# Performance work log

Measured on AMD Instinct MI355X. Metric: run time of the kernel, lower is better.

Reference implementation:

```python
import jax, jax.numpy as jnp
import numpy as np

B, T, C, H, W = 2, 4, 3, 96, 96
HF, L = 128, 6
TC = T * C
EPS = 1e-5


def swish(x):
    return x * jax.nn.sigmoid(x)


def _build_edges(h, w):
    # self-loops + 8-neighbor grid edges, exactly as image_to_graph
    edges = [np.stack([np.arange(h * w)] * 2)]
    nx0, ny0 = np.meshgrid(np.arange(w), np.arange(h), indexing='ij')
    for dx, dy in [(-1, -1), (0, -1), (1, -1), (-1, 0), (1, 0), (-1, 1), (0, 1), (1, 1)]:
        nx, ny = nx0 + dx, ny0 + dy
        src = ny * w + nx
        dst = (ny - dy) * w + (nx - dx)
        ok = (nx >= 0) & (nx < w) & (0 <= ny) & (ny < h)
        edges.append(np.stack([src[ok], dst[ok]]))
    return np.concatenate(edges, axis=1)


def setup_inputs() -> dict:
    key = jax.random.key(0)
    ks = iter(jax.random.split(key, 40))

    def lin(fi, fo):
        return jax.random.normal(next(ks), (fi, fo), jnp.float32) / np.sqrt(fi).astype(np.float32)

    x = jax.random.normal(next(ks), (B, T, C, H, W), jnp.float32)
    ei = _build_edges(H, W)
    px, py = np.meshgrid(np.arange(W), np.arange(H), indexing='ij')
    pos = np.stack([px.flatten(), py.flatten()], 1).astype(np.float32) / (H - 1)
    return dict(
        x=x,
        edge_src=jnp.asarray(ei[0], jnp.int32),
        edge_dst=jnp.asarray(ei[1], jnp.int32),
        pos=jnp.asarray(pos),
        emb_w1=lin(TC + 2, HF), emb_b1=jnp.zeros((HF,), jnp.float32),
        emb_w2=lin(HF, HF), emb_b2=jnp.zeros((HF,), jnp.float32),
        msg_w1=jnp.stack([lin(2 * HF + TC + 1, HF) for _ in range(L)]),
        msg_b1=jnp.zeros((L, HF), jnp.float32),
        msg_w2=jnp.stack([lin(HF, HF) for _ in range(L)]),
        msg_b2=jnp.zeros((L, HF), jnp.float32),
        upd_w1=jnp.stack([lin(2 * HF, HF) for _ in range(L)]),
        upd_b1=jnp.zeros((L, HF), jnp.float32),
        upd_w2=jnp.stack([lin(HF, HF) for _ in range(L)]),
        upd_b2=jnp.zeros((L, HF), jnp.float32),
        out_w1=lin(HF, HF), out_b1=jnp.zeros((HF,), jnp.float32),
        out_w2=lin(HF, C), out_b2=jnp.zeros((C,), jnp.float32),
    )


def _forward(x, emb_w1, emb_b1, emb_w2, emb_b2, msg_w1, msg_b1, msg_w2, msg_b2,
             upd_w1, upd_b1, upd_w2, upd_b2, out_w1, out_b1, out_w2, out_b2,
             edge_src, edge_dst, pos):
    b, t, c, h, w = x.shape
    n = h * w
    u = x.reshape(b, t * c, n).transpose(0, 2, 1)                       # [B,N,TC]
    node_in = jnp.concatenate([u, jnp.broadcast_to(pos, (b, n, 2))], -1)
    hf = swish(swish(node_in @ emb_w1 + emb_b1) @ emb_w2 + emb_b2)      # [B,N,HF]
    dist = jnp.linalg.norm(pos[edge_dst] - pos[edge_src], axis=1, keepdims=True)  # [E,1]
    dist_b = jnp.broadcast_to(dist, (b,) + dist.shape)
    deg = jnp.zeros((n,), x.dtype).at[edge_dst].add(1.0)                # >=1 (self loops)
    for l in range(msg_w1.shape[0]):
        m_in = jnp.concatenate([hf[:, edge_dst], hf[:, edge_src],
                                u[:, edge_dst] - u[:, edge_src], dist_b], -1)
        m = swish(swish(m_in @ msg_w1[l] + msg_b1[l]) @ msg_w2[l] + msg_b2[l])
        agg = jnp.zeros(hf.shape, hf.dtype).at[:, edge_dst].add(m) / deg[None, :, None]
        upd = swish(swish(jnp.concatenate([hf, agg], -1) @ upd_w1[l] + upd_b1[l])
                    @ upd_w2[l] + upd_b2[l])
        hf = hf + upd                                                    # residual (in==out)
        mu = hf.mean(axis=1, keepdims=True)                              # InstanceNorm per graph
        var = hf.var(axis=1, keepdims=True)
        hf = (hf - mu) * jax.lax.rsqrt(var + EPS)
    hg = hf.reshape(b, h, w, -1)
    diff = (swish(hg @ out_w1 + out_b1) @ out_w2 + out_b2).transpose(0, 3, 1, 2)
    return (x[:, -1] + diff)[:, None]                                    # [B,1,C,H,W]


def reference(x, edge_src, edge_dst, pos, emb_w1, emb_b1, emb_w2, emb_b2,
              msg_w1, msg_b1, msg_w2, msg_b2, upd_w1, upd_b1, upd_w2, upd_b2,
              out_w1, out_b1, out_w2, out_b2):
    return _forward(x, emb_w1, emb_b1, emb_w2, emb_b2, msg_w1, msg_b1, msg_w2, msg_b2,
                    upd_w1, upd_b1, upd_w2, upd_b2, out_w1, out_b1, out_w2, out_b2,
                    edge_src, edge_dst, pos)
```

## Files before the change

kernel.cpp:

```cpp
#include <hip/hip_runtime.h>
#include <math.h>

#define HF 128
#define NB 9216
#define BB 2
#define MROWS (BB*NB)
#define GH 96
#define GW 96
#define LAYERS 6

typedef __attribute__((ext_vector_type(8))) short bf16x8;
typedef __attribute__((ext_vector_type(4))) float f32x4;

#define MFMA16(a, b, c) __builtin_amdgcn_mfma_f32_16x16x32_bf16(a, b, c, 0, 0, 0)

__device__ __forceinline__ float swishf(float x) {
    return __fdividef(x, 1.0f + __expf(-x));
}

__device__ __forceinline__ unsigned short f2b(float f) {
    unsigned u = __float_as_uint(f);
    unsigned r = (u + 0x7fffu + ((u >> 16) & 1u)) >> 16;
    return (unsigned short)r;
}
__device__ __forceinline__ float b2f(unsigned short u) {
    return __uint_as_float((unsigned)u << 16);
}

__global__ void k_prep(const float* __restrict__ embw2, const float* __restrict__ outw1,
                       const float* __restrict__ msgw1, const float* __restrict__ msgw2,
                       const float* __restrict__ updw1, const float* __restrict__ updw2,
                       unsigned short* __restrict__ wT) {
    int s = blockIdx.x;
    const float* src;
    if (s == 0) src = embw2;
    else if (s == 1) src = outw1;
    else {
        int l = (s - 2) / 6, r = (s - 2) % 6;
        if (r == 0)      src = msgw1 + (size_t)l * 269 * HF;
        else if (r == 1) src = msgw1 + (size_t)l * 269 * HF + HF * HF;
        else if (r == 2) src = msgw2 + (size_t)l * HF * HF;
        else if (r == 3) src = updw1 + (size_t)l * 256 * HF;
        else if (r == 4) src = updw1 + (size_t)l * 256 * HF + HF * HF;
        else             src = updw2 + (size_t)l * HF * HF;
    }
    __shared__ float tile[128][133];
    int t = threadIdx.x;
#pragma unroll
    for (int i = 0; i < 64; ++i) {
        int id = i * 256 + t;
        tile[id >> 7][id & 127] = src[id];
    }
    __syncthreads();
    unsigned short* o = wT + (size_t)s * 16384;
#pragma unroll
    for (int i = 0; i < 64; ++i) {
        int id = i * 256 + t;
        int col = id >> 7, k = id & 127;
        o[id] = f2b(tile[k][col]);
    }
}

__global__ void k_build(const float* __restrict__ x, const float* __restrict__ pos,
                        float* __restrict__ nodein) {
    int idx = blockIdx.x * 256 + threadIdx.x;
    if (idx >= MROWS) return;
    int b = idx / NB, n = idx - b * NB;
    float* o = nodein + (size_t)idx * 16;
    const float* xb = x + (size_t)b * 12 * NB + n;
#pragma unroll
    for (int k = 0; k < 12; ++k) o[k] = xb[(size_t)k * NB];
    o[12] = pos[2 * n];
    o[13] = pos[2 * n + 1];
    o[14] = 0.0f; o[15] = 0.0f;
}

__global__ __launch_bounds__(256, 4)
void k_emb(const float* __restrict__ nodein, const float* __restrict__ w1,
           const float* __restrict__ b1, const unsigned short* __restrict__ wT2,
           const float* __restrict__ b2,
           float* __restrict__ hf, unsigned short* __restrict__ hfb) {
    __shared__ float xs[16][14];
    __shared__ char t1s[4096];
    int t = threadIdx.x;
    int rt = blockIdx.x * 16;
    if (t < 224) {
        int r = t / 14, k = t - r * 14;
        xs[r][k] = nodein[(size_t)(rt + r) * 16 + k];
    }
    __syncthreads();
    {
        int f = t & 127, rblk = t >> 7;
        float wreg[14];
#pragma unroll
        for (int k = 0; k < 14; ++k) wreg[k] = w1[k * HF + f];
        float bv = b1[f];
#pragma unroll
        for (int i = 0; i < 8; ++i) {
            int row = rblk * 8 + i;
            float acc = bv;
#pragma unroll
            for (int k = 0; k < 14; ++k) acc = fmaf(xs[row][k], wreg[k], acc);
            int addr = (row * 256 + f * 2) ^ ((row & 7) << 4);
            *(unsigned short*)(t1s + addr) = f2b(swishf(acc));
        }
    }
    __syncthreads();
    int wave = t >> 6, lane = t & 63, lr = lane & 15, lg = lane >> 4;
    int fb = wave * 32;
    f32x4 acc[2];
    acc[0] = (f32x4)0.0f; acc[1] = (f32x4)0.0f;
#pragma unroll
    for (int kc = 0; kc < 4; ++kc) {
        int k0 = kc * 32 + lg * 8;
        bf16x8 a = *(const bf16x8*)(t1s + ((lr * 256 + k0 * 2) ^ ((lr & 7) << 4)));
#pragma unroll
        for (int j = 0; j < 2; ++j) {
            bf16x8 b = *(const bf16x8*)(wT2 + (size_t)(fb + j * 16 + lr) * HF + k0);
            acc[j] = MFMA16(a, b, acc[j]);
        }
    }
#pragma unroll
    for (int j = 0; j < 2; ++j) {
        int f = fb + j * 16 + lr;
        float bv = b2[f];
#pragma unroll
        for (int r = 0; r < 4; ++r) {
            size_t o = (size_t)(rt + lg * 4 + r) * HF + f;
            float v = swishf(acc[j][r] + bv);
            hf[o] = v;
            hfb[o] = f2b(v);
        }
    }
}

__global__ __launch_bounds__(256, 4)
void k_as(const unsigned short* __restrict__ hfb, const unsigned short* __restrict__ wA,
          const unsigned short* __restrict__ wB, const float* __restrict__ nodein,
          const float* __restrict__ w1u,
          unsigned short* __restrict__ A, unsigned short* __restrict__ S) {
    __shared__ float w1s[12][128];
    int t = threadIdx.x, wave = t >> 6, lane = t & 63, lr = lane & 15, lg = lane >> 4;
    int rt = blockIdx.x * 16;
    int fb = wave * 32;
    for (int i = t; i < 12 * 128; i += 256) w1s[i >> 7][i & 127] = w1u[i];
    f32x4 accA[2], accS[2];
    accA[0] = (f32x4)0.0f; accA[1] = (f32x4)0.0f;
    accS[0] = (f32x4)0.0f; accS[1] = (f32x4)0.0f;
#pragma unroll
    for (int kc = 0; kc < 4; ++kc) {
        int k0 = kc * 32 + lg * 8;
        bf16x8 a = *(const bf16x8*)(hfb + (size_t)(rt + lr) * HF + k0);
#pragma unroll
        for (int j = 0; j < 2; ++j) {
            bf16x8 bA = *(const bf16x8*)(wA + (size_t)(fb + j * 16 + lr) * HF + k0);
            accA[j] = MFMA16(a, bA, accA[j]);
            bf16x8 bS = *(const bf16x8*)(wB + (size_t)(fb + j * 16 + lr) * HF + k0);
            accS[j] = MFMA16(a, bS, accS[j]);
        }
    }
    float ni[4][12];
#pragma unroll
    for (int r = 0; r < 4; ++r) {
        const float4* np = (const float4*)(nodein + (size_t)(rt + lg * 4 + r) * 16);
        float4 v0 = np[0], v1 = np[1], v2 = np[2];
        ni[r][0] = v0.x; ni[r][1] = v0.y; ni[r][2] = v0.z; ni[r][3] = v0.w;
        ni[r][4] = v1.x; ni[r][5] = v1.y; ni[r][6] = v1.z; ni[r][7] = v1.w;
        ni[r][8] = v2.x; ni[r][9] = v2.y; ni[r][10] = v2.z; ni[r][11] = v2.w;
    }
    __syncthreads();
#pragma unroll
    for (int j = 0; j < 2; ++j) {
        int f = fb + j * 16 + lr;
        float au[4] = {0.f, 0.f, 0.f, 0.f};
#pragma unroll
        for (int k = 0; k < 12; ++k) {
            float wv = w1s[k][f];
#pragma unroll
            for (int r = 0; r < 4; ++r) au[r] = fmaf(ni[r][k], wv, au[r]);
        }
#pragma unroll
        for (int r = 0; r < 4; ++r) {
            size_t o = (size_t)(rt + lg * 4 + r) * HF + f;
            A[o] = f2b(accA[j][r] + au[r]);
            S[o] = f2b(accS[j][r] - au[r]);
        }
    }
}

__global__ __launch_bounds__(256, 4)
void k_agg(const unsigned short* __restrict__ Ab, const unsigned short* __restrict__ Sb,
           const unsigned short* __restrict__ wT2, const float* __restrict__ b2,
           const float* __restrict__ b1, const float* __restrict__ w1d,
           unsigned short* __restrict__ aggb) {
    __shared__ float dsb[3][128];
    __shared__ char exb[9 * 4096];
    int t = threadIdx.x, kq = t >> 6, lane = t & 63, lr = lane & 15, lg = lane >> 4;
    int bx = blockIdx.x;
    int b = bx / (NB / 16), tile = bx % (NB / 16);
    int rt = tile * 16;
    int fb = kq * 32;
    size_t bN = (size_t)b * NB;
    int R = rt / GW, C0 = rt % GW;

    if (t < 128) {
        float bb = b1[t], wd = w1d[t];
        dsb[0][t] = bb;
        dsb[1][t] = fmaf(1.0f / 95.0f, wd, bb);
        dsb[2][t] = fmaf(1.4142135623730951f / 95.0f, wd, bb);
    }
    bf16x8 w2f[2][4];
#pragma unroll
    for (int j = 0; j < 2; ++j)
#pragma unroll
        for (int kc = 0; kc < 4; ++kc)
            w2f[j][kc] = *(const bf16x8*)(wT2 + (size_t)(fb + j * 16 + lr) * HF
                                          + kc * 32 + lg * 8);
    int rowA = rt + lr;
    float Af[8];
    {
        bf16x8 av = *(const bf16x8*)(Ab + (bN + rowA) * HF + kq * 32 + lg * 8);
#pragma unroll
        for (int e = 0; e < 8; ++e) Af[e] = b2f((unsigned short)av[e]);
    }
    float b2r[2] = { b2[fb + lr], b2[fb + 16 + lr] };
    int lofs = lane * 16;
    __syncthreads();

    bf16x8 sv;
    {
        int src = min(max(rowA - 97, 0), NB - 1);
        sv = *(const bf16x8*)(Sb + (bN + src) * HF + kq * 32 + lg * 8);
    }
#pragma unroll
    for (int off = 0; off < 9; ++off) {
        int dr = off / 3 - 1, dc = off % 3 - 1;
        int dd = dr * dr + dc * dc;
        bf16x8 cur = sv;
        if (off < 8) {
            int no = off + 1;
            int dnn = (no / 3 - 1) * GW + (no % 3 - 1);
            int src = min(max(rowA + dnn, 0), NB - 1);
            sv = *(const bf16x8*)(Sb + (bN + src) * HF + kq * 32 + lg * 8);
        }
        const float* dp = &dsb[dd][kq * 32 + lg * 8];
        union { bf16x8 v; unsigned u[4]; } az;
#pragma unroll
        for (int q = 0; q < 4; ++q) {
            float zl = swishf(Af[2 * q]     + b2f((unsigned short)cur[2 * q])     + dp[2 * q]);
            float zh = swishf(Af[2 * q + 1] + b2f((unsigned short)cur[2 * q + 1]) + dp[2 * q + 1]);
            az.u[q] = (unsigned)f2b(zl) | ((unsigned)f2b(zh) << 16);
        }
        *(bf16x8*)(exb + off * 4096 + kq * 1024 + lofs) = az.v;
    }
    __syncthreads();

    f32x4 agg2[2];
    agg2[0] = (f32x4)0.0f; agg2[1] = (f32x4)0.0f;
#pragma unroll
    for (int off = 0; off < 9; ++off) {
        int dr = off / 3 - 1, dc = off % 3 - 1;
        f32x4 acc[2];
        acc[0] = (f32x4)0.0f; acc[1] = (f32x4)0.0f;
#pragma unroll
        for (int kc = 0; kc < 4; ++kc) {
            bf16x8 a = *(const bf16x8*)(exb + off * 4096 + kc * 1024 + lofs);
            acc[0] = MFMA16(a, w2f[0][kc], acc[0]);
            acc[1] = MFMA16(a, w2f[1][kc], acc[1]);
        }
        bool rOK = (unsigned)(R + dr) < (unsigned)GH;
#pragma unroll
        for (int j = 0; j < 2; ++j)
#pragma unroll
            for (int r = 0; r < 4; ++r) {
                int C = C0 + lg * 4 + r;
                if (rOK && (unsigned)(C + dc) < (unsigned)GW)
                    agg2[j][r] += swishf(acc[j][r] + b2r[j]);
            }
    }
    float nr = 1.0f + (R > 0) + (R < GH - 1);
#pragma unroll
    for (int j = 0; j < 2; ++j)
#pragma unroll
        for (int r = 0; r < 4; ++r) {
            int n = rt + lg * 4 + r;
            int C = C0 + lg * 4 + r;
            float nc = 1.0f + (C > 0) + (C < GW - 1);
            aggb[(bN + n) * HF + fb + j * 16 + lr] =
                f2b(__fdividef(agg2[j][r], nr * nc));
        }
}

__global__ __launch_bounds__(256, 4)
void k_upd(const unsigned short* __restrict__ hfb_in, const unsigned short* __restrict__ aggb,
           const unsigned short* __restrict__ w1a, const unsigned short* __restrict__ w1b,
           const unsigned short* __restrict__ w2, const float* __restrict__ b1v,
           const float* __restrict__ b2v, float* __restrict__ hf,
           unsigned short* __restrict__ hfb_out, float* __restrict__ partial) {
    __shared__ char t1s[4096];
    int t = threadIdx.x, wave = t >> 6, lane = t & 63, lr = lane & 15, lg = lane >> 4;
    int rt = blockIdx.x * 16;
    int fb = wave * 32;
    f32x4 acc[2];
    acc[0] = (f32x4)0.0f; acc[1] = (f32x4)0.0f;
#pragma unroll
    for (int kc = 0; kc < 4; ++kc) {
        int k0 = kc * 32 + lg * 8;
        bf16x8 a1 = *(const bf16x8*)(hfb_in + (size_t)(rt + lr) * HF + k0);
        bf16x8 a2 = *(const bf16x8*)(aggb + (size_t)(rt + lr) * HF + k0);
#pragma unroll
        for (int j = 0; j < 2; ++j) {
            bf16x8 bA = *(const bf16x8*)(w1a + (size_t)(fb + j * 16 + lr) * HF + k0);
            acc[j] = MFMA16(a1, bA, acc[j]);
            bf16x8 bB = *(const bf16x8*)(w1b + (size_t)(fb + j * 16 + lr) * HF + k0);
            acc[j] = MFMA16(a2, bB, acc[j]);
        }
    }
#pragma unroll
    for (int j = 0; j < 2; ++j) {
        int col = fb + j * 16 + lr;
        float bv = b1v[col];
#pragma unroll
        for (int r = 0; r < 4; ++r) {
            int row = lg * 4 + r;
            int addr = (row * 256 + col * 2) ^ ((row & 7) << 4);
            *(unsigned short*)(t1s + addr) = f2b(swishf(acc[j][r] + bv));
        }
    }
    __syncthreads();
    f32x4 acc2[2];
    acc2[0] = (f32x4)0.0f; acc2[1] = (f32x4)0.0f;
#pragma unroll
    for (int kc = 0; kc < 4; ++kc) {
        int k0 = kc * 32 + lg * 8;
        bf16x8 a = *(const bf16x8*)(t1s + ((lr * 256 + k0 * 2) ^ ((lr & 7) << 4)));
#pragma unroll
        for (int j = 0; j < 2; ++j) {
            bf16x8 b = *(const bf16x8*)(w2 + (size_t)(fb + j * 16 + lr) * HF + k0);
            acc2[j] = MFMA16(a, b, acc2[j]);
        }
    }
#pragma unroll
    for (int j = 0; j < 2; ++j) {
        int f = fb + j * 16 + lr;
        float bv = b2v[f];
        float s1 = 0.f, s2 = 0.f;
#pragma unroll
        for (int r = 0; r < 4; ++r) {
            size_t o = (size_t)(rt + lg * 4 + r) * HF + f;
            float v = swishf(acc2[j][r] + bv) + hf[o];
            hf[o] = v;
            hfb_out[o] = f2b(v);
            s1 += v; s2 += v * v;
        }
        s1 += __shfl_xor(s1, 16); s1 += __shfl_xor(s1, 32);
        s2 += __shfl_xor(s2, 16); s2 += __shfl_xor(s2, 32);
        if (lg == 0) {
            float* p = partial + ((size_t)blockIdx.x * HF + f) * 2;
            p[0] = s1; p[1] = s2;
        }
    }
}

__global__ void k_stats(const float* __restrict__ partial, float* __restrict__ musig) {
    __shared__ float ss[256], qq[256];
    int bx = blockIdx.x;
    int b = bx >> 7, f = bx & 127;
    int t = threadIdx.x;
    float s = 0.f, q = 0.f;
    for (int i = t; i < 576; i += 256) {
        const float* p = partial + (((size_t)(b * 576 + i)) * HF + f) * 2;
        s += p[0]; q += p[1];
    }
    ss[t] = s; qq[t] = q;
    __syncthreads();
    for (int st = 128; st > 0; st >>= 1) {
        if (t < st) { ss[t] += ss[t + st]; qq[t] += qq[t + st]; }
        __syncthreads();
    }
    if (t == 0) {
        float mu = ss[0] * (1.0f / NB);
        float var = qq[0] * (1.0f / NB) - mu * mu;
        musig[bx] = mu;
        musig[256 + bx] = rsqrtf(var + 1e-5f);
    }
}

__global__ void k_norm(float* __restrict__ hf, const float* __restrict__ musig,
                       unsigned short* __restrict__ hfb) {
    int idx = blockIdx.x * 256 + threadIdx.x;
    if (idx >= MROWS * HF / 4) return;
    int b = (idx >= NB * HF / 4) ? 1 : 0;
    int f = (idx * 4) & 127;
    float4 v = ((const float4*)hf)[idx];
    const float* mu = musig + b * 128 + f;
    const float* rs = musig + 256 + b * 128 + f;
    v.x = (v.x - mu[0]) * rs[0];
    v.y = (v.y - mu[1]) * rs[1];
    v.z = (v.z - mu[2]) * rs[2];
    v.w = (v.w - mu[3]) * rs[3];
    ((float4*)hf)[idx] = v;
    uint2 p;
    p.x = (unsigned)f2b(v.x) | ((unsigned)f2b(v.y) << 16);
    p.y = (unsigned)f2b(v.z) | ((unsigned)f2b(v.w) << 16);
    *(uint2*)(hfb + (size_t)idx * 4) = p;
}

__global__ __launch_bounds__(256, 4)
void k_out(const unsigned short* __restrict__ hfb, const unsigned short* __restrict__ wT1,
           const float* __restrict__ b1, const float* __restrict__ w2,
           const float* __restrict__ b2, const float* __restrict__ x,
           float* __restrict__ out) {
    __shared__ float g1s[16][132];
    __shared__ float w2s[384];
    int t = threadIdx.x, wave = t >> 6, lane = t & 63, lr = lane & 15, lg = lane >> 4;
    int rt = blockIdx.x * 16;
    int fb = wave * 32;
    for (int i = t; i < 384; i += 256) w2s[i] = w2[i];
    f32x4 acc[2];
    acc[0] = (f32x4)0.0f; acc[1] = (f32x4)0.0f;
#pragma unroll
    for (int kc = 0; kc < 4; ++kc) {
        int k0 = kc * 32 + lg * 8;
        bf16x8 a = *(const bf16x8*)(hfb + (size_t)(rt + lr) * HF + k0);
#pragma unroll
        for (int j = 0; j < 2; ++j) {
            bf16x8 b = *(const bf16x8*)(wT1 + (size_t)(fb + j * 16 + lr) * HF + k0);
            acc[j] = MFMA16(a, b, acc[j]);
        }
    }
#pragma unroll
    for (int j = 0; j < 2; ++j) {
        int f = fb + j * 16 + lr;
        float bv = b1[f];
#pragma unroll
        for (int r = 0; r < 4; ++r)
            g1s[lg * 4 + r][f] = swishf(acc[j][r] + bv);
    }
    __syncthreads();
    if (t < 48) {
        int r = t / 3, c = t - (t / 3) * 3;
        int row = rt + r;
        int b = row / NB, n = row - b * NB;
        float a = b2[c];
#pragma unroll 8
        for (int k = 0; k < HF; ++k) a = fmaf(g1s[r][k], w2s[k * 3 + c], a);
        float xv = x[(((size_t)b * 4 + 3) * 3 + c) * NB + n];
        out[((size_t)b * 3 + c) * NB + n] = a + xv;
    }
}

extern "C" void kernel_launch(void* const* d_in, const int* in_sizes, int n_in,
                              void* d_out, int out_size, void* d_ws, size_t ws_size,
                              hipStream_t stream) {
    const float* x      = (const float*)d_in[0];
    const float* pos    = (const float*)d_in[3];
    const float* emb_w1 = (const float*)d_in[4];
    const float* emb_b1 = (const float*)d_in[5];
    const float* emb_b2 = (const float*)d_in[7];
    const float* msg_w1 = (const float*)d_in[8];
    const float* msg_b1 = (const float*)d_in[9];
    const float* msg_b2 = (const float*)d_in[11];
    const float* upd_b1 = (const float*)d_in[13];
    const float* upd_b2 = (const float*)d_in[15];
    const float* out_b1 = (const float*)d_in[17];
    const float* out_w2 = (const float*)d_in[18];
    const float* out_b2 = (const float*)d_in[19];

    float* w = (float*)d_ws;
    size_t off = 0;
    auto alloc = [&](size_t n) { float* p = w + off; off += n; return p; };
    float* nodein  = alloc((size_t)MROWS * 16);
    float* hf      = alloc((size_t)MROWS * HF);
    float* partial = alloc((size_t)1152 * HF * 2);
    float* musig   = alloc(512);
    unsigned short* hfb  = (unsigned short*)alloc((size_t)MROWS * 64);
    unsigned short* aggb = (unsigned short*)alloc((size_t)MROWS * 64);
    unsigned short* Abf  = (unsigned short*)alloc((size_t)MROWS * 64);
    unsigned short* Sbf  = (unsigned short*)alloc((size_t)MROWS * 64);
    unsigned short* wT   = (unsigned short*)alloc((size_t)38 * 16384 / 2);
    (void)ws_size; (void)in_sizes; (void)n_in; (void)out_size;

    k_prep<<<38, 256, 0, stream>>>((const float*)d_in[6], (const float*)d_in[16],
                                   msg_w1, (const float*)d_in[10],
                                   (const float*)d_in[12], (const float*)d_in[14], wT);
    k_build<<<(MROWS + 255) / 256, 256, 0, stream>>>(x, pos, nodein);
    k_emb<<<1152, 256, 0, stream>>>(nodein, emb_w1, emb_b1, wT + 0 * 16384, emb_b2,
                                    hf, hfb);
    for (int l = 0; l < LAYERS; ++l) {
        const unsigned short* wL = wT + (size_t)(2 + 6 * l) * 16384;
        const float* W1 = msg_w1 + (size_t)l * 269 * HF;
        k_as<<<1152, 256, 0, stream>>>(hfb, wL + 0 * 16384, wL + 1 * 16384,
                                       nodein, W1 + 256 * HF, Abf, Sbf);
        k_agg<<<1152, 256, 0, stream>>>(Abf, Sbf, wL + 2 * 16384, msg_b2 + l * HF,
                                        msg_b1 + l * HF, W1 + 268 * HF, aggb);
        k_upd<<<1152, 256, 0, stream>>>(hfb, aggb, wL + 3 * 16384, wL + 4 * 16384,
                                        wL + 5 * 16384, upd_b1 + l * HF,
                                        upd_b2 + l * HF, hf, hfb, partial);
        k_stats<<<256, 256, 0, stream>>>(partial, musig);
        k_norm<<<(MROWS * HF / 4 + 255) / 256, 256, 0, stream>>>(hf, musig, hfb);
    }
    k_out<<<1152, 256, 0, stream>>>(hfb, wT + 1 * 16384, out_b1, out_w2, out_b2,
                                    x, (float*)d_out);
}
```

Baseline: 550.1 us.

## Fuse instance-norm apply into consumer kernels and drop separate norm pass

Removes the k_norm kernel and the bf16 copy of hidden features. Consumers (k_as, k_upd, k_out) now read fp32 hf and apply the pending mean/rstd normalization on the fly when building MFMA fragments, with musig initialized to identity for the first layer. This cuts one kernel launch and a full read/write pass per layer, but the GEMM A-operand loads become fp32 (twice the bytes) and need extra arithmetic and conversion.

```diff
diff --git a/kernel.cpp b/kernel.cpp
--- a/kernel.cpp
+++ b/kernel.cpp
@@ -25,6 +25,27 @@
 }
 __device__ __forceinline__ float b2f(unsigned short u) {
     return __uint_as_float((unsigned)u << 16);
+}
+
+__device__ __forceinline__ bf16x8 norm_frag(const float* __restrict__ hp,
+                                            const float* __restrict__ mus,
+                                            const float* __restrict__ rss, int k0) {
+    float4 h0 = *(const float4*)hp;
+    float4 h1 = *(const float4*)(hp + 4);
+    float4 m0 = *(const float4*)&mus[k0];
+    float4 m1 = *(const float4*)&mus[k0 + 4];
+    float4 r0 = *(const float4*)&rss[k0];
+    float4 r1 = *(const float4*)&rss[k0 + 4];
+    union { bf16x8 v; unsigned u[4]; } az;
+    float a0 = (h0.x - m0.x) * r0.x, a1 = (h0.y - m0.y) * r0.y;
+    az.u[0] = (unsigned)f2b(a0) | ((unsigned)f2b(a1) << 16);
+    float a2 = (h0.z - m0.z) * r0.z, a3 = (h0.w - m0.w) * r0.w;
+    az.u[1] = (unsigned)f2b(a2) | ((unsigned)f2b(a3) << 16);
+    float a4 = (h1.x - m1.x) * r1.x, a5 = (h1.y - m1.y) * r1.y;
+    az.u[2] = (unsigned)f2b(a4) | ((unsigned)f2b(a5) << 16);
+    float a6 = (h1.z - m1.z) * r1.z, a7 = (h1.w - m1.w) * r1.w;
+    az.u[3] = (unsigned)f2b(a6) | ((unsigned)f2b(a7) << 16);
+    return az.v;
 }
 
 __global__ void k_prep(const float* __restrict__ embw2, const float* __restrict__ outw1,
@@ -62,8 +83,13 @@
 }
 
 __global__ void k_build(const float* __restrict__ x, const float* __restrict__ pos,
-                        float* __restrict__ nodein) {
-    int idx = blockIdx.x * 256 + threadIdx.x;
+                        float* __restrict__ nodein, float* __restrict__ musig) {
+    int t = threadIdx.x;
+    int idx = blockIdx.x * 256 + t;
+    if (blockIdx.x == 0 && t < 256) {
+        musig[t] = 0.0f;
+        musig[256 + t] = 1.0f;
+    }
     if (idx >= MROWS) return;
     int b = idx / NB, n = idx - b * NB;
     float* o = nodein + (size_t)idx * 16;
@@ -78,8 +104,7 @@
 __global__ __launch_bounds__(256, 4)
 void k_emb(const float* __restrict__ nodein, const float* __restrict__ w1,
            const float* __restrict__ b1, const unsigned short* __restrict__ wT2,
-           const float* __restrict__ b2,
-           float* __restrict__ hf, unsigned short* __restrict__ hfb) {
+           const float* __restrict__ b2, float* __restrict__ hf) {
     __shared__ float xs[16][14];
     __shared__ char t1s[4096];
     int t = threadIdx.x;
@@ -127,30 +152,32 @@
 #pragma unroll
         for (int r = 0; r < 4; ++r) {
             size_t o = (size_t)(rt + lg * 4 + r) * HF + f;
-            float v = swishf(acc[j][r] + bv);
-            hf[o] = v;
-            hfb[o] = f2b(v);
+            hf[o] = swishf(acc[j][r] + bv);
         }
     }
 }
 
 __global__ __launch_bounds__(256, 4)
-void k_as(const unsigned short* __restrict__ hfb, const unsigned short* __restrict__ wA,
-          const unsigned short* __restrict__ wB, const float* __restrict__ nodein,
-          const float* __restrict__ w1u,
+void k_as(const float* __restrict__ hf, const float* __restrict__ musig,
+          const unsigned short* __restrict__ wA, const unsigned short* __restrict__ wB,
+          const float* __restrict__ nodein, const float* __restrict__ w1u,
           unsigned short* __restrict__ A, unsigned short* __restrict__ S) {
     __shared__ float w1s[12][128];
+    __shared__ float mus[128], rss[128];
     int t = threadIdx.x, wave = t >> 6, lane = t & 63, lr = lane & 15, lg = lane >> 4;
     int rt = blockIdx.x * 16;
+    int b = blockIdx.x / (NB / 16);
     int fb = wave * 32;
     for (int i = t; i < 12 * 128; i += 256) w1s[i >> 7][i & 127] = w1u[i];
+    if (t < 128) { mus[t] = musig[b * 128 + t]; rss[t] = musig[256 + b * 128 + t]; }
+    __syncthreads();
     f32x4 accA[2], accS[2];
     accA[0] = (f32x4)0.0f; accA[1] = (f32x4)0.0f;
     accS[0] = (f32x4)0.0f; accS[1] = (f32x4)0.0f;
 #pragma unroll
     for (int kc = 0; kc < 4; ++kc) {
         int k0 = kc * 32 + lg * 8;
-        bf16x8 a = *(const bf16x8*)(hfb + (size_t)(rt + lr) * HF + k0);
+        bf16x8 a = norm_frag(hf + (size_t)(rt + lr) * HF + k0, mus, rss, k0);
 #pragma unroll
         for (int j = 0; j < 2; ++j) {
             bf16x8 bA = *(const bf16x8*)(wA + (size_t)(fb + j * 16 + lr) * HF + k0);
@@ -168,7 +195,6 @@
         ni[r][4] = v1.x; ni[r][5] = v1.y; ni[r][6] = v1.z; ni[r][7] = v1.w;
         ni[r][8] = v2.x; ni[r][9] = v2.y; ni[r][10] = v2.z; ni[r][11] = v2.w;
     }
-    __syncthreads();
 #pragma unroll
     for (int j = 0; j < 2; ++j) {
         int f = fb + j * 16 + lr;
@@ -292,21 +318,25 @@
 }
 
 __global__ __launch_bounds__(256, 4)
-void k_upd(const unsigned short* __restrict__ hfb_in, const unsigned short* __restrict__ aggb,
+void k_upd(float* __restrict__ hf, const float* __restrict__ musig,
+           const unsigned short* __restrict__ aggb,
            const unsigned short* __restrict__ w1a, const unsigned short* __restrict__ w1b,
            const unsigned short* __restrict__ w2, const float* __restrict__ b1v,
-           const float* __restrict__ b2v, float* __restrict__ hf,
-           unsigned short* __restrict__ hfb_out, float* __restrict__ partial) {
+           const float* __restrict__ b2v, float* __restrict__ partial) {
     __shared__ char t1s[4096];
+    __shared__ float mus[128], rss[128];
     int t = threadIdx.x, wave = t >> 6, lane = t & 63, lr = lane & 15, lg = lane >> 4;
     int rt = blockIdx.x * 16;
+    int b = blockIdx.x / (NB / 16);
     int fb = wave * 32;
+    if (t < 128) { mus[t] = musig[b * 128 + t]; rss[t] = musig[256 + b * 128 + t]; }
+    __syncthreads();
     f32x4 acc[2];
     acc[0] = (f32x4)0.0f; acc[1] = (f32x4)0.0f;
 #pragma unroll
     for (int kc = 0; kc < 4; ++kc) {
         int k0 = kc * 32 + lg * 8;
-        bf16x8 a1 = *(const bf16x8*)(hfb_in + (size_t)(rt + lr) * HF + k0);
+        bf16x8 a1 = norm_frag(hf + (size_t)(rt + lr) * HF + k0, mus, rss, k0);
         bf16x8 a2 = *(const bf16x8*)(aggb + (size_t)(rt + lr) * HF + k0);
 #pragma unroll
         for (int j = 0; j < 2; ++j) {
@@ -344,13 +374,13 @@
     for (int j = 0; j < 2; ++j) {
         int f = fb + j * 16 + lr;
         float bv = b2v[f];
+        float mu = mus[f], rs = rss[f];
         float s1 = 0.f, s2 = 0.f;
 #pragma unroll
         for (int r = 0; r < 4; ++r) {
             size_t o = (size_t)(rt + lg * 4 + r) * HF + f;
-            float v = swishf(acc2[j][r] + bv) + hf[o];
+            float v = swishf(acc2[j][r] + bv) + (hf[o] - mu) * rs;
             hf[o] = v;
-            hfb_out[o] = f2b(v);
             s1 += v; s2 += v * v;
         }
         s1 += __shfl_xor(s1, 16); s1 += __shfl_xor(s1, 32);
@@ -386,47 +416,31 @@
     }
 }
 
-__global__ void k_norm(float* __restrict__ hf, const float* __restrict__ musig,
-                       unsigned short* __restrict__ hfb) {
-    int idx = blockIdx.x * 256 + threadIdx.x;
-    if (idx >= MROWS * HF / 4) return;
-    int b = (idx >= NB * HF / 4) ? 1 : 0;
-    int f = (idx * 4) & 127;
-    float4 v = ((const float4*)hf)[idx];
-    const float* mu = musig + b * 128 + f;
-    const float* rs = musig + 256 + b * 128 + f;
-    v.x = (v.x - mu[0]) * rs[0];
-    v.y = (v.y - mu[1]) * rs[1];
-    v.z = (v.z - mu[2]) * rs[2];
-    v.w = (v.w - mu[3]) * rs[3];
-    ((float4*)hf)[idx] = v;
-    uint2 p;
-    p.x = (unsigned)f2b(v.x) | ((unsigned)f2b(v.y) << 16);
-    p.y = (unsigned)f2b(v.z) | ((unsigned)f2b(v.w) << 16);
-    *(uint2*)(hfb + (size_t)idx * 4) = p;
-}
-
 __global__ __launch_bounds__(256, 4)
-void k_out(const unsigned short* __restrict__ hfb, const unsigned short* __restrict__ wT1,
-           const float* __restrict__ b1, const float* __restrict__ w2,
-           const float* __restrict__ b2, const float* __restrict__ x,
-           float* __restrict__ out) {
+void k_out(const float* __restrict__ hf, const float* __restrict__ musig,
+           const unsigned short* __restrict__ wT1, const float* __restrict__ b1,
+           const float* __restrict__ w2, const float* __restrict__ b2,
+           const float* __restrict__ x, float* __restrict__ out) {
     __shared__ float g1s[16][132];
     __shared__ float w2s[384];
+    __shared__ float mus[128], rss[128];
     int t = threadIdx.x, wave = t >> 6, lane = t & 63, lr = lane & 15, lg = lane >> 4;
     int rt = blockIdx.x * 16;
+    int b = blockIdx.x / (NB / 16);
     int fb = wave * 32;
     for (int i = t; i < 384; i += 256) w2s[i] = w2[i];
+    if (t < 128) { mus[t] = musig[b * 128 + t]; rss[t] = musig[256 + b * 128 + t]; }
+    __syncthreads();
     f32x4 acc[2];
     acc[0] = (f32x4)0.0f; acc[1] = (f32x4)0.0f;
 #pragma unroll
     for (int kc = 0; kc < 4; ++kc) {
         int k0 = kc * 32 + lg * 8;
-        bf16x8 a = *(const bf16x8*)(hfb + (size_t)(rt + lr) * HF + k0);
+        bf16x8 a = norm_frag(hf + (size_t)(rt + lr) * HF + k0, mus, rss, k0);
 #pragma unroll
         for (int j = 0; j < 2; ++j) {
-            bf16x8 b = *(const bf16x8*)(wT1 + (size_t)(fb + j * 16 + lr) * HF + k0);
-            acc[j] = MFMA16(a, b, acc[j]);
+            bf16x8 bfr = *(const bf16x8*)(wT1 + (size_t)(fb + j * 16 + lr) * HF + k0);
+            acc[j] = MFMA16(a, bfr, acc[j]);
         }
     }
 #pragma unroll
@@ -441,12 +455,12 @@
     if (t < 48) {
         int r = t / 3, c = t - (t / 3) * 3;
         int row = rt + r;
-        int b = row / NB, n = row - b * NB;
+        int bb = row / NB, n = row - bb * NB;
         float a = b2[c];
 #pragma unroll 8
         for (int k = 0; k < HF; ++k) a = fmaf(g1s[r][k], w2s[k * 3 + c], a);
-        float xv = x[(((size_t)b * 4 + 3) * 3 + c) * NB + n];
-        out[((size_t)b * 3 + c) * NB + n] = a + xv;
+        float xv = x[(((size_t)bb * 4 + 3) * 3 + c) * NB + n];
+        out[((size_t)bb * 3 + c) * NB + n] = a + xv;
     }
 }
 
@@ -474,7 +488,6 @@
     float* hf      = alloc((size_t)MROWS * HF);
     float* partial = alloc((size_t)1152 * HF * 2);
     float* musig   = alloc(512);
-    unsigned short* hfb  = (unsigned short*)alloc((size_t)MROWS * 64);
     unsigned short* aggb = (unsigned short*)alloc((size_t)MROWS * 64);
     unsigned short* Abf  = (unsigned short*)alloc((size_t)MROWS * 64);
     unsigned short* Sbf  = (unsigned short*)alloc((size_t)MROWS * 64);
@@ -484,22 +497,20 @@
     k_prep<<<38, 256, 0, stream>>>((const float*)d_in[6], (const float*)d_in[16],
                                    msg_w1, (const float*)d_in[10],
                                    (const float*)d_in[12], (const float*)d_in[14], wT);
-    k_build<<<(MROWS + 255) / 256, 256, 0, stream>>>(x, pos, nodein);
-    k_emb<<<1152, 256, 0, stream>>>(nodein, emb_w1, emb_b1, wT + 0 * 16384, emb_b2,
-                                    hf, hfb);
+    k_build<<<(MROWS + 255) / 256, 256, 0, stream>>>(x, pos, nodein, musig);
+    k_emb<<<1152, 256, 0, stream>>>(nodein, emb_w1, emb_b1, wT + 0 * 16384, emb_b2, hf);
     for (int l = 0; l < LAYERS; ++l) {
         const unsigned short* wL = wT + (size_t)(2 + 6 * l) * 16384;
         const float* W1 = msg_w1 + (size_t)l * 269 * HF;
-        k_as<<<1152, 256, 0, stream>>>(hfb, wL + 0 * 16384, wL + 1 * 16384,
+        k_as<<<1152, 256, 0, stream>>>(hf, musig, wL + 0 * 16384, wL + 1 * 16384,
                                        nodein, W1 + 256 * HF, Abf, Sbf);
         k_agg<<<1152, 256, 0, stream>>>(Abf, Sbf, wL + 2 * 16384, msg_b2 + l * HF,
                                         msg_b1 + l * HF, W1 + 268 * HF, aggb);
-        k_upd<<<1152, 256, 0, stream>>>(hfb, aggb, wL + 3 * 16384, wL + 4 * 16384,
+        k_upd<<<1152, 256, 0, stream>>>(hf, musig, aggb, wL + 3 * 16384, wL + 4 * 16384,
                                         wL + 5 * 16384, upd_b1 + l * HF,
-                                        upd_b2 + l * HF, hf, hfb, partial);
+                                        upd_b2 + l * HF, partial);
         k_stats<<<256, 256, 0, stream>>>(partial, musig);
-        k_norm<<<(MROWS * HF / 4 + 255) / 256, 256, 0, stream>>>(hf, musig, hfb);
-    }
-    k_out<<<1152, 256, 0, stream>>>(hfb, wT + 1 * 16384, out_b1, out_w2, out_b2,
+    }
+    k_out<<<1152, 256, 0, stream>>>(hf, musig, wT + 1 * 16384, out_b1, out_w2, out_b2,
                                     x, (float*)d_out);
 }
```

Result: faster. 522.8 us (-5.0%).
